# Kernel optimization log

Measured on AMD Instinct MI355X. Metric: run time of the kernel, lower is better.

Reference implementation:

```python
import jax, jax.numpy as jnp
import numpy as np

NUM_HEADS = 4

def _pos_encoding(seq_len, d, dtype):
    # standard sinusoidal positional encoding [seq_len, d]
    pos = jnp.arange(seq_len, dtype=jnp.float32)[:, None]
    i = jnp.arange(0, d, 2, dtype=jnp.float32)
    div = jnp.exp(-jnp.log(10000.0) * i / d)
    ang = pos * div
    pe = jnp.zeros((seq_len, d), jnp.float32)
    pe = pe.at[:, 0::2].set(jnp.sin(ang)).at[:, 1::2].set(jnp.cos(ang))
    return pe.astype(dtype)

def _layer_norm(x, g, b, eps=1e-5):
    m = jnp.mean(x, axis=-1, keepdims=True)
    v = jnp.mean(jnp.square(x - m), axis=-1, keepdims=True)
    return (x - m) / jnp.sqrt(v + eps) * g + b

def setup_inputs() -> dict:
    key = jax.random.key(0)
    ks = jax.random.split(key, 10)
    B, S, H, W, N = 8, 512, 768, 8, 4096
    s = 0.02
    token_reps = jax.random.normal(ks[0], (B, S, H), jnp.float32)
    starts = jax.random.randint(ks[1], (B, N), 0, S - W)
    widths = jax.random.randint(ks[2], (B, N), 1, W + 1)
    span_ids = jnp.stack([starts, starts + widths], axis=-1)  # end > start, end <= S
    span_masks = jax.random.randint(ks[3], (B, N), 0, 2)
    return dict(
        token_reps=token_reps,
        dummy_query=jax.random.normal(ks[4], (H,), jnp.float32) * s,
        in_proj_w=jax.random.normal(ks[5], (3 * H, H), jnp.float32) * s,
        in_proj_b=jnp.zeros((3 * H,), jnp.float32),
        out_w=jax.random.normal(ks[6], (H, H), jnp.float32) * s,
        out_b=jnp.zeros((H,), jnp.float32),
        ln_g=jnp.ones((H,), jnp.float32),
        ln_b=jnp.zeros((H,), jnp.float32),
        ffn_w1=jax.random.normal(ks[7], (H, 4 * H), jnp.float32) * s,
        ffn_b1=jnp.zeros((4 * H,), jnp.float32),
        ffn_w2=jax.random.normal(ks[8], (4 * H, H), jnp.float32) * s,
        ffn_b2=jnp.zeros((H,), jnp.float32),
        span_ids=span_ids,
        span_masks=span_masks,
    )

def reference(token_reps, dummy_query, in_proj_w, in_proj_b, out_w, out_b,
              ln_g, ln_b, ffn_w1, ffn_b1, ffn_w2, ffn_b2, span_ids, span_masks):
    B, S, H = token_reps.shape
    N = span_ids.shape[1]
    NH = NUM_HEADS
    DH = H // NH
    # sequence positional encoding (dropout is identity in eval mode)
    x = token_reps + _pos_encoding(S, H, token_reps.dtype)[None]
    Wq, Wk, Wv = jnp.split(in_proj_w, 3, axis=0)
    bq, bk, bv = jnp.split(in_proj_b, 3)
    # single shared dummy query -> per-head query [NH, DH]
    q = (dummy_query @ Wq.T + bq).reshape(NH, DH)
    k = (x @ Wk.T + bk).reshape(B, S, NH, DH)
    v = (x @ Wv.T + bv).reshape(B, S, NH, DH)
    # scores are identical across spans since the query is shared: [B, NH, S]
    scores = jnp.einsum('hd,bshd->bhs', q, k) / jnp.sqrt(jnp.asarray(DH, x.dtype))
    pos = jnp.arange(S)
    # per-span key validity: start <= pos < end, and span not masked out  [B, N, S]
    valid = (pos[None, None, :] >= span_ids[..., 0:1]) & \
            (pos[None, None, :] < span_ids[..., 1:2]) & \
            (span_masks[..., None] != 0)
    logits = jnp.where(valid[:, :, None, :], scores[:, None, :, :], -1e9)  # [B,N,NH,S]
    w = jax.nn.softmax(logits, axis=-1)
    attn = jnp.einsum('bnhs,bshd->bnhd', w, v).reshape(B, N, H)
    attn = attn @ out_w.T + out_b
    h1 = _layer_norm(attn + dummy_query, ln_g, ln_b)
    ffn = jax.nn.relu(h1 @ ffn_w1 + ffn_b1) @ ffn_w2 + ffn_b2
    out = _layer_norm(ffn + h1, ln_g, ln_b)
    # masked spans produce exact zeros, matching the original loop
    return out * (span_masks[..., None] != 0).astype(out.dtype)
```

## Files before the change

### kernel.cpp

```cpp
#include <hip/hip_runtime.h>
#include <hip/hip_bf16.h>

#define Bb 8
#define Ss 512
#define Hh 768
#define NHh 4
#define Nn 4096
#define ROWS (Bb * Nn)
#define SCB 128

typedef _Float16 f16x8 __attribute__((ext_vector_type(8)));
typedef _Float16 f16x4 __attribute__((ext_vector_type(4)));
typedef _Float16 f16x2 __attribute__((ext_vector_type(2)));
typedef float f32x4 __attribute__((ext_vector_type(4)));

#define DEVINL __device__ __forceinline__

DEVINL void gld_lds16(const void* g, void* l) {
  __builtin_amdgcn_global_load_lds(
      (const __attribute__((address_space(1))) void*)g,
      (__attribute__((address_space(3))) void*)l, 16, 0, 0);
}

template <int V>
DEVINL void wait_vmcnt() {
  if constexpr (V == 0) asm volatile("s_waitcnt vmcnt(0)" ::: "memory");
  else if constexpr (V == 3) asm volatile("s_waitcnt vmcnt(3)" ::: "memory");
  else if constexpr (V == 4) asm volatile("s_waitcnt vmcnt(4)" ::: "memory");
  else if constexpr (V == 6) asm volatile("s_waitcnt vmcnt(6)" ::: "memory");
  else if constexpr (V == 8) asm volatile("s_waitcnt vmcnt(8)" ::: "memory");
}

DEVINL float block_sum256(float v, float* red) {
#pragma unroll
  for (int o = 32; o; o >>= 1) v += __shfl_xor(v, o, 64);
  const int wid = threadIdx.x >> 6, lane = threadIdx.x & 63;
  if (lane == 0) red[wid] = v;
  __syncthreads();
  float r = red[0] + red[1] + red[2] + red[3];
  __syncthreads();
  return r;
}

__global__ __launch_bounds__(256) void x_kernel(const float* __restrict__ tok,
                                                _Float16* __restrict__ x) {
  int idx = blockIdx.x * 256 + threadIdx.x;
  int t = idx % 384;
  int bs = idx / 384;
  int s = bs & (Ss - 1);
  float div = expf(-(float)t * 0.02398526138535465f);
  float ang = (float)s * div;
  float sv = sinf(ang), cv = cosf(ang);
  const float2 tv = ((const float2*)tok)[(size_t)bs * 384 + t];
  f16x2 o;
  o[0] = (_Float16)(tv.x + sv);
  o[1] = (_Float16)(tv.y + cv);
  *(f16x2*)&x[(size_t)bs * Hh + 2 * t] = o;
}

__global__ __launch_bounds__(256) void q_kernel(const float* __restrict__ dq,
                                                const float* __restrict__ ipw,
                                                const float* __restrict__ ipb,
                                                float* __restrict__ qout) {
  __shared__ float red[4];
  int o = blockIdx.x;
  const float* wr = ipw + (size_t)o * Hh;
  float s = 0.f;
#pragma unroll
  for (int e = 0; e < 3; e++) {
    int j = threadIdx.x + 256 * e;
    s += dq[j] * wr[j];
  }
  s = block_sum256(s, red);
  if (threadIdx.x == 0) qout[o] = s + ipb[o];
}

__global__ __launch_bounds__(256) void c_kernel(const float* __restrict__ q,
                                                const float* __restrict__ ipw,
                                                const float* __restrict__ ipb,
                                                float* __restrict__ cout,
                                                float* __restrict__ sbias) {
  __shared__ float red[4];
  int bid = blockIdx.x;
  int t = threadIdx.x;
  if (bid < 3072) {
    int h = bid / Hh;
    int j = bid - h * Hh;
    float s = 0.f;
    if (t < 192) s = q[h * 192 + t] * ipw[(size_t)(Hh + h * 192 + t) * Hh + j];
    s = block_sum256(s, red);
    if (t == 0) cout[bid] = s;
  } else {
    int h = bid - 3072;
    float s = 0.f;
    if (t < 192) s = q[h * 192 + t] * ipb[Hh + h * 192 + t];
    s = block_sum256(s, red);
    if (t == 0) sbias[h] = s;
  }
}

__global__ __launch_bounds__(256) void score_kernel(
    const _Float16* __restrict__ x, const float* __restrict__ c,
    const float* __restrict__ sbias, float* __restrict__ scores) {
  int bs = blockIdx.x;
  int wid = threadIdx.x >> 6, lane = threadIdx.x & 63;
  const _Float16* xr = x + (size_t)bs * Hh;
  const float* ch = c + wid * Hh;
  float s = 0.f;
#pragma unroll
  for (int e = 0; e < 12; e++) {
    int j = e * 64 + lane;
    s += (float)xr[j] * ch[j];
  }
#pragma unroll
  for (int o = 32; o; o >>= 1) s += __shfl_xor(s, o, 64);
  if (lane == 0) {
    int b = bs >> 9, pos = bs & (Ss - 1);
    scores[((size_t)(b * NHh + wid)) * Ss + pos] =
        (s + sbias[wid]) * 0.07216878364870322f;
  }
}

__global__ __launch_bounds__(256) void cvt_kernel(const float* __restrict__ in,
                                                  _Float16* __restrict__ out) {
  int i = blockIdx.x * 256 + threadIdx.x;
  float4 f = ((const float4*)in)[i];
  f16x4 o;
  o[0] = (_Float16)f.x;
  o[1] = (_Float16)f.y;
  o[2] = (_Float16)f.z;
  o[3] = (_Float16)f.w;
  ((f16x4*)out)[i] = o;
}

__global__ __launch_bounds__(256) void trcvt_kernel(const float* __restrict__ in,
                                                    _Float16* __restrict__ out,
                                                    int R, int C) {
  __shared__ float tile[32][33];
  int c0 = blockIdx.x * 32, r0 = blockIdx.y * 32;
  int tx = threadIdx.x & 31, ty0 = threadIdx.x >> 5;
#pragma unroll
  for (int ty = ty0; ty < 32; ty += 8)
    tile[ty][tx] = in[(size_t)(r0 + ty) * C + c0 + tx];
  __syncthreads();
#pragma unroll
  for (int ty = ty0; ty < 32; ty += 8)
    out[(size_t)(c0 + ty) * R + r0 + tx] = (_Float16)tile[tx][ty];
}

__global__ __launch_bounds__(256) void scan1_kernel(const int* __restrict__ mask,
                                                    int* __restrict__ bsum) {
  int r = blockIdx.x * 256 + threadIdx.x;
  unsigned long long b = __ballot(mask[r] != 0);
  __shared__ int wsum[4];
  int lane = threadIdx.x & 63, wid = threadIdx.x >> 6;
  if (lane == 0) wsum[wid] = __popcll(b);
  __syncthreads();
  if (threadIdx.x == 0)
    bsum[blockIdx.x] = wsum[0] + wsum[1] + wsum[2] + wsum[3];
}
__global__ __launch_bounds__(64) void scan2_kernel(const int* __restrict__ bsum,
                                                   int* __restrict__ boff,
                                                   int* __restrict__ cnt) {
  if (threadIdx.x == 0) {
    int acc = 0;
    for (int i = 0; i < SCB; i++) {
      boff[i] = acc;
      acc += bsum[i];
    }
    *cnt = acc;
  }
}
__global__ __launch_bounds__(256) void cidx_kernel(const int* __restrict__ mask,
                                                   const int* __restrict__ boff,
                                                   int* __restrict__ cidx) {
  int r = blockIdx.x * 256 + threadIdx.x;
  int m = mask[r] != 0;
  unsigned long long b = __ballot(m);
  __shared__ int wsum[4];
  int lane = threadIdx.x & 63, wid = threadIdx.x >> 6;
  if (lane == 0) wsum[wid] = __popcll(b);
  __syncthreads();
  int pre = 0;
#pragma unroll
  for (int i = 0; i < 3; i++)
    if (i < wid) pre += wsum[i];
  pre += __popcll(b & ((1ULL << lane) - 1));
  if (m) cidx[r] = boff[blockIdx.x] + pre;
}

#define PIPE_LOOP(LPSV)                                   \
  const int nt = K >> 5;                                  \
  STAGE(0, 0);                                            \
  STAGE(1, 32);                                           \
  int t = 0;                                              \
  for (; t <= nt - 6; t += 3) {                           \
    wait_vmcnt<LPSV>();                                   \
    __builtin_amdgcn_s_barrier();                         \
    STAGE(2, (t + 2) * 32);                               \
    COMPUTE(0);                                           \
    wait_vmcnt<LPSV>();                                   \
    __builtin_amdgcn_s_barrier();                         \
    STAGE(0, (t + 3) * 32);                               \
    COMPUTE(1);                                           \
    wait_vmcnt<LPSV>();                                   \
    __builtin_amdgcn_s_barrier();                         \
    STAGE(1, (t + 4) * 32);                               \
    COMPUTE(2);                                           \
  }                                                       \
    \
  wait_vmcnt<LPSV>();                                     \
  __builtin_amdgcn_s_barrier();                           \
  STAGE(2, (nt - 1) * 32);                                \
  COMPUTE(0);                                             \
  wait_vmcnt<LPSV>();                                     \
  __builtin_amdgcn_s_barrier();                           \
  COMPUTE(1);                                             \
  wait_vmcnt<0>();                                        \
  __builtin_amdgcn_s_barrier();                           \
  COMPUTE(2);

template <int RELU, int BN>
__global__ __launch_bounds__(256, 2) void gemm_nt(
    const _Float16* __restrict__ A, const _Float16* __restrict__ W,
    const float* __restrict__ bias, _Float16* __restrict__ C, int N, int K,
    int nn, const int* __restrict__ mcount) {
  const int bid = (int)blockIdx.x;
  const int mi = (bid >> 3) / nn;
  const int nt_ = (bid >> 3) - mi * nn;
  const long m0 = (long)(mi * 8 + (bid & 7)) * 128;
  const long n0 = (long)nt_ * BN;
  if (mcount && m0 >= (long)*mcount) return;
  __shared__ __align__(16) _Float16 As[3][128 * 32];
  __shared__ __align__(16) _Float16 Bs[3][BN * 32];
  const int tid = threadIdx.x;
  const int wid = tid >> 6;
  const int lane = tid & 63;
  constexpr int LPS = (BN == 128) ? 4 : 3;

  const int c0 = wid * 64 + lane;
  const int c1 = c0 + 256;
  const int sw0 = ((c0 & 3) ^ ((c0 >> 3) & 3)) * 8;
  const int sw1 = ((c1 & 3) ^ ((c1 >> 3) & 3)) * 8;
  const _Float16* gA0 = A + (m0 + (c0 >> 2)) * K + sw0;
  const _Float16* gA1 = A + (m0 + (c1 >> 2)) * K + sw1;
  const _Float16* gB0 = W + (n0 + (c0 >> 2)) * K + sw0;
  const _Float16* gB1 = W + (n0 + (c1 >> 2)) * K + sw1;

  const int wr = (wid >> 1) * 64;
  const int wc = (wid & 1) * (BN / 2);
  constexpr int NF = BN / 32;
  const int fr = lane & 15;
  const int fkb = lane >> 4;

  f32x4 acc[4][NF];
#pragma unroll
  for (int mi2 = 0; mi2 < 4; mi2++)
#pragma unroll
    for (int ni = 0; ni < NF; ni++) acc[mi2][ni] = (f32x4){0.f, 0.f, 0.f, 0.f};

#define STAGE(buf, k0)                                                  \
  do {                                                                  \
    gld_lds16(gA0 + (k0), &As[buf][wid * 512]);                         \
    gld_lds16(gA1 + (k0), &As[buf][2048 + wid * 512]);                  \
    gld_lds16(gB0 + (k0), &Bs[buf][wid * 512]);                         \
    if constexpr (BN == 128) gld_lds16(gB1 + (k0), &Bs[buf][2048 + wid * 512]); \
  } while (0)

#define COMPUTE(buf)                                                          \
  do {                                                                        \
    f16x8 af[4], bf[NF];                                                      \
    _Pragma("unroll") for (int i = 0; i < 4; i++) {                           \
      int r_ = wr + i * 16 + fr;                                              \
      af[i] = *(const f16x8*)&As[buf][r_ * 32 + ((fkb ^ ((r_ >> 1) & 3)) * 8)]; \
    }                                                                         \
    _Pragma("unroll") for (int i = 0; i < NF; i++) {                          \
      int r_ = wc + i * 16 + fr;                                              \
      bf[i] = *(const f16x8*)&Bs[buf][r_ * 32 + ((fkb ^ ((r_ >> 1) & 3)) * 8)]; \
    }                                                                         \
    __builtin_amdgcn_s_setprio(1);                                            \
    _Pragma("unroll") for (int mi2 = 0; mi2 < 4; mi2++)                       \
        _Pragma("unroll") for (int ni = 0; ni < NF; ni++)                     \
            acc[mi2][ni] = __builtin_amdgcn_mfma_f32_16x16x32_f16(            \
                af[mi2], bf[ni], acc[mi2][ni], 0, 0, 0);                      \
    __builtin_amdgcn_s_setprio(0);                                            \
  } while (0)

  PIPE_LOOP(LPS)
#undef STAGE
#undef COMPUTE

  const int crow = (lane >> 4) * 4;
  const int ccol = lane & 15;
  float bv[NF];
#pragma unroll
  for (int ni = 0; ni < NF; ni++)
    bv[ni] = bias ? bias[n0 + wc + ni * 16 + ccol] : 0.f;
#pragma unroll
  for (int mi2 = 0; mi2 < 4; mi2++)
#pragma unroll
    for (int ni = 0; ni < NF; ni++)
#pragma unroll
      for (int i = 0; i < 4; i++) {
        float v = acc[mi2][ni][i] + bv[ni];
        if (RELU) v = fmaxf(v, 0.f);
        C[(m0 + wr + mi2 * 16 + crow + i) * (long)N + (n0 + wc + ni * 16 + ccol)] =
            (_Float16)v;
      }
}

template <int RELU>
__global__ __launch_bounds__(512, 4) void gemm8_nt(
    const _Float16* __restrict__ A, const _Float16* __restrict__ W,
    const float* __restrict__ bias, _Float16* __restrict__ C, int N, int K,
    int nn, const int* __restrict__ mcount) {
  const int bid = (int)blockIdx.x;
  const int mi = (bid >> 3) / nn;
  const int nt_ = (bid >> 3) - mi * nn;
  const long m0 = (long)(mi * 8 + (bid & 7)) * 256;
  const long n0 = (long)nt_ * 128;
  if (mcount && m0 >= (long)*mcount) return;
  __shared__ __align__(16) _Float16 As[3][256 * 32];
  __shared__ __align__(16) _Float16 Bs[3][128 * 32];
  const int tid = threadIdx.x;
  const int w = tid >> 6;
  const int lane = tid & 63;
  constexpr int LPS = 3;

  const int rA0 = w * 16 + (lane >> 2);
  const int rA1 = rA0 + 128;
  const int cb = lane & 3;
  const int swA0 = (cb ^ ((rA0 >> 1) & 3)) * 8;
  const int swA1 = (cb ^ ((rA1 >> 1) & 3)) * 8;
  const _Float16* gA0 = A + (m0 + rA0) * K + swA0;
  const _Float16* gA1 = A + (m0 + rA1) * K + swA1;
  const _Float16* gB0 = W + (n0 + rA0) * K + swA0;

  const int wr = (w >> 1) * 64;
  const int wc = (w & 1) * 64;
  const int fr = lane & 15;
  const int fkb = lane >> 4;

  f32x4 acc[4][4];
#pragma unroll
  for (int mi2 = 0; mi2 < 4; mi2++)
#pragma unroll
    for (int ni = 0; ni < 4; ni++) acc[mi2][ni] = (f32x4){0.f, 0.f, 0.f, 0.f};

#define STAGE(buf, k0)                                   \
  do {                                                   \
    gld_lds16(gA0 + (k0), &As[buf][w * 512]);            \
    gld_lds16(gA1 + (k0), &As[buf][(w + 8) * 512]);      \
    gld_lds16(gB0 + (k0), &Bs[buf][w * 512]);            \
  } while (0)

#define COMPUTE(buf)                                                          \
  do {                                                                        \
    f16x8 af[4], bf[4];                                                       \
    _Pragma("unroll") for (int i = 0; i < 4; i++) {                           \
      int r_ = wr + i * 16 + fr;                                              \
      af[i] = *(const f16x8*)&As[buf][r_ * 32 + ((fkb ^ ((r_ >> 1) & 3)) * 8)]; \
    }                                                                         \
    _Pragma("unroll") for (int i = 0; i < 4; i++) {                           \
      int r_ = wc + i * 16 + fr;                                              \
      bf[i] = *(const f16x8*)&Bs[buf][r_ * 32 + ((fkb ^ ((r_ >> 1) & 3)) * 8)]; \
    }                                                                         \
    __builtin_amdgcn_s_setprio(1);                                            \
    _Pragma("unroll") for (int mi2 = 0; mi2 < 4; mi2++)                       \
        _Pragma("unroll") for (int ni = 0; ni < 4; ni++)                      \
            acc[mi2][ni] = __builtin_amdgcn_mfma_f32_16x16x32_f16(            \
                af[mi2], bf[ni], acc[mi2][ni], 0, 0, 0);                      \
    __builtin_amdgcn_s_setprio(0);                                            \
  } while (0)

  PIPE_LOOP(LPS)
#undef STAGE
#undef COMPUTE

  const int crow = (lane >> 4) * 4;
  const int ccol = lane & 15;
  float bv[4];
#pragma unroll
  for (int ni = 0; ni < 4; ni++)
    bv[ni] = bias ? bias[n0 + wc + ni * 16 + ccol] : 0.f;
#pragma unroll
  for (int mi2 = 0; mi2 < 4; mi2++)
#pragma unroll
    for (int ni = 0; ni < 4; ni++)
#pragma unroll
      for (int i = 0; i < 4; i++) {
        float v = acc[mi2][ni][i] + bv[ni];
        if (RELU) v = fmaxf(v, 0.f);
        C[(m0 + wr + mi2 * 16 + crow + i) * (long)N + (n0 + wc + ni * 16 + ccol)] =
            (_Float16)v;
      }
}

__global__ __launch_bounds__(192) void pool_kernel(
    const _Float16* __restrict__ v, const float* __restrict__ scores,
    const int* __restrict__ span_ids, const int* __restrict__ span_masks,
    _Float16* __restrict__ attn, const int* __restrict__ cidx) {
  int r = blockIdx.x;
  if (span_masks[r] == 0) return;
  int slot = cidx[r];
  int i = threadIdx.x;
  int h = i / 48;
  int d0 = i * 4;
  int b = r >> 12;
  int st = span_ids[2 * r], en = span_ids[2 * r + 1];
  int wdt = en - st;
  const float* sc = scores + ((size_t)(b * NHh + h)) * Ss + st;
  float w[8];
  float mx = -1e30f;
#pragma unroll
  for (int j = 0; j < 8; j++) {
    float t = (j < wdt) ? sc[j] : -1e30f;
    w[j] = t;
    mx = fmaxf(mx, t);
  }
  float sum = 0.f;
#pragma unroll
  for (int j = 0; j < 8; j++) {
    float e = (j < wdt) ? expf(w[j] - mx) : 0.f;
    w[j] = e;
    sum += e;
  }
  float inv = 1.f / sum;
  float a0 = 0.f, a1 = 0.f, a2 = 0.f, a3 = 0.f;
#pragma unroll
  for (int j = 0; j < 8; j++) {
    if (j < wdt) {
      f16x4 vv = *(const f16x4*)(v + ((size_t)(b * Ss + st + j)) * Hh + d0);
      float wj = w[j] * inv;
      a0 += wj * (float)vv[0];
      a1 += wj * (float)vv[1];
      a2 += wj * (float)vv[2];
      a3 += wj * (float)vv[3];
    }
  }
  f16x4 o;
  o[0] = (_Float16)a0;
  o[1] = (_Float16)a1;
  o[2] = (_Float16)a2;
  o[3] = (_Float16)a3;
  *(f16x4*)&attn[(size_t)slot * Hh + d0] = o;
}

__global__ __launch_bounds__(256) void ln0_kernel(
    _Float16* __restrict__ X, const float* __restrict__ AddV,
    const float* __restrict__ g, const float* __restrict__ bta,
    const int* __restrict__ mcount) {
  __shared__ float red[4];
  int r = blockIdx.x;
  if (r >= *mcount) return;
  int t = threadIdx.x;
  float xv[3];
#pragma unroll
  for (int e = 0; e < 3; e++) {
    int d = t + 256 * e;
    xv[e] = (float)X[(size_t)r * Hh + d] + AddV[d];
  }
  float s = xv[0] + xv[1] + xv[2];
  s = block_sum256(s, red);
  float mean = s * (1.f / 768.f);
  float vs = 0.f;
#pragma unroll
  for (int e = 0; e < 3; e++) {
    float d = xv[e] - mean;
    vs += d * d;
  }
  vs = block_sum256(vs, red);
  float inv = rsqrtf(vs * (1.f / 768.f) + 1e-5f);
#pragma unroll
  for (int e = 0; e < 3; e++) {
    int d = t + 256 * e;
    X[(size_t)r * Hh + d] = (_Float16)((xv[e] - mean) * inv * g[d] + bta[d]);
  }
}

__global__ __launch_bounds__(256) void ln1_kernel(
    const _Float16* __restrict__ F2c, const _Float16* __restrict__ h1c,
    const int* __restrict__ cidx, const float* __restrict__ g,
    const float* __restrict__ bta, const int* __restrict__ mask,
    float* __restrict__ out) {
  __shared__ float red[4];
  int r = blockIdx.x;
  int t = threadIdx.x;
  float* orow = out + (size_t)r * Hh;
  if (mask[r] == 0) {
#pragma unroll
    for (int e = 0; e < 3; e++) orow[t + 256 * e] = 0.f;
    return;
  }
  int c = cidx[r];
  float xv[3];
#pragma unroll
  for (int e = 0; e < 3; e++) {
    int d = t + 256 * e;
    xv[e] = (float)F2c[(size_t)c * Hh + d] + (float)h1c[(size_t)c * Hh + d];
  }
  float s = xv[0] + xv[1] + xv[2];
  s = block_sum256(s, red);
  float mean = s * (1.f / 768.f);
  float vs = 0.f;
#pragma unroll
  for (int e = 0; e < 3; e++) {
    float d = xv[e] - mean;
    vs += d * d;
  }
  vs = block_sum256(vs, red);
  float inv = rsqrtf(vs * (1.f / 768.f) + 1e-5f);
#pragma unroll
  for (int e = 0; e < 3; e++) {
    int d = t + 256 * e;
    orow[d] = (xv[e] - mean) * inv * g[d] + bta[d];
  }
}

extern "C" void kernel_launch(void* const* d_in, const int* in_sizes, int n_in,
                              void* d_out, int out_size, void* d_ws,
                              size_t ws_size, hipStream_t stream) {
  (void)out_size;
  if (n_in != 14) return;
  if (in_sizes[0] != 3145728 || in_sizes[2] != 1769472 ||
      in_sizes[3] != 2304 || in_sizes[4] != 589824 ||
      in_sizes[8] != 2359296 || in_sizes[9] != 3072 ||
      in_sizes[12] != 65536 || in_sizes[13] != 32768)
    return;

  const float* tok   = (const float*)d_in[0];
  const float* dq    = (const float*)d_in[1];
  const float* ipw   = (const float*)d_in[2];
  const float* ipb   = (const float*)d_in[3];
  const float* outw  = (const float*)d_in[4];
  const float* outb  = (const float*)d_in[5];
  const float* lng   = (const float*)d_in[6];
  const float* lnb   = (const float*)d_in[7];
  const float* w1    = (const float*)d_in[8];
  const float* b1    = (const float*)d_in[9];
  const float* w2    = (const float*)d_in[10];
  const float* b2    = (const float*)d_in[11];
  const int* spid    = (const int*)d_in[12];
  const int* spmask  = (const int*)d_in[13];

  char* ws = (char*)d_ws;
  size_t off = 0;
  auto alloc = [&](size_t bytes) {
    size_t r = off;
    off = (off + bytes + 255) & ~(size_t)255;
    return r;
  };
  _Float16* X16  = (_Float16*)(ws + alloc((size_t)Bb * Ss * Hh * 2));
  float* SC      = (float*)(ws + alloc((size_t)Bb * NHh * Ss * 4));
  float* Q       = (float*)(ws + alloc(768 * 4));
  float* Cc      = (float*)(ws + alloc(3072 * 4));
  float* SB      = (float*)(ws + alloc(4 * 4));
  _Float16* WV16 = (_Float16*)(ws + alloc((size_t)768 * 768 * 2));
  _Float16* OW16 = (_Float16*)(ws + alloc((size_t)768 * 768 * 2));
  _Float16* WT1  = (_Float16*)(ws + alloc((size_t)3072 * 768 * 2));
  _Float16* WT2  = (_Float16*)(ws + alloc((size_t)768 * 3072 * 2));
  _Float16* ATTN = (_Float16*)(ws + alloc((size_t)ROWS * Hh * 2));
  _Float16* PROJ = (_Float16*)(ws + alloc((size_t)ROWS * Hh * 2));
  _Float16* F1   = (_Float16*)(ws + alloc((size_t)ROWS * 3072 * 2));
  if (ws_size < off) return;
  _Float16* F2 = ATTN;

  int* CIDX = (int*)X16;
  int* BSUM = (int*)X16 + ROWS;
  int* BOFF = (int*)X16 + ROWS + SCB;
  int* CNT  = (int*)X16 + ROWS + 2 * SCB;

  _Float16* V16 = (_Float16*)d_out;

  cvt_kernel<<<576, 256, 0, stream>>>(ipw + (size_t)1536 * 768, WV16);
  cvt_kernel<<<576, 256, 0, stream>>>(outw, OW16);
  trcvt_kernel<<<dim3(96, 24), 256, 0, stream>>>(w1, WT1, 768, 3072);
  trcvt_kernel<<<dim3(24, 96), 256, 0, stream>>>(w2, WT2, 3072, 768);

  x_kernel<<<(Bb * Ss * 384) / 256, 256, 0, stream>>>(tok, X16);
  q_kernel<<<768, 256, 0, stream>>>(dq, ipw, ipb, Q);
  c_kernel<<<3076, 256, 0, stream>>>(Q, ipw, ipb, Cc, SB);
  score_kernel<<<Bb * Ss, 256, 0, stream>>>(X16, Cc, SB, SC);
  gemm_nt<0, 64><<<384, 256, 0, stream>>>(X16, WV16, ipb + 1536, V16,
                                          768, 768, 12, nullptr);
  scan1_kernel<<<SCB, 256, 0, stream>>>(spmask, BSUM);
  scan2_kernel<<<1, 64, 0, stream>>>(BSUM, BOFF, CNT);
  cidx_kernel<<<SCB, 256, 0, stream>>>(spmask, BOFF, CIDX);
  pool_kernel<<<ROWS, 192, 0, stream>>>(V16, SC, spid, spmask, ATTN, CIDX);
  gemm8_nt<0><<<768, 512, 0, stream>>>(ATTN, OW16, outb, PROJ,
                                       768, 768, 6, CNT);
  ln0_kernel<<<ROWS, 256, 0, stream>>>(PROJ, dq, lng, lnb, CNT);
  gemm8_nt<1><<<3072, 512, 0, stream>>>(PROJ, WT1, b1, F1,
                                        3072, 768, 24, CNT);
  gemm8_nt<0><<<768, 512, 0, stream>>>(F1, WT2, b2, F2,
                                       768, 3072, 6, CNT);
  ln1_kernel<<<ROWS, 256, 0, stream>>>(F2, PROJ, CIDX, lng, lnb, spmask,
                                       (float*)d_out);
}
```

Baseline: 372.2 us.

## Split-K the narrow GEMMs, chunk the FFN over rows, restructure the LDS pipeline

The out-projection and FFN2 GEMMs, which have only 768 output columns, now use a two-way split-K. The grid doubles, and each half writes a partial fp16 result to its own buffer. The partials are summed inside the following layer-norm kernels. The FFN runs in two row chunks of 16384 rows so the F1 intermediate buffer is halved and more likely to stay in cache. The software pipeline now prefetches three stages and restages each buffer after computing it. This adds fp16 partial-sum rounding, extra launches, and another barrier per iteration.

```diff
diff --git a/kernel.cpp b/kernel.cpp
--- a/kernel.cpp
+++ b/kernel.cpp
@@ -8,6 +8,7 @@
 #define Nn 4096
 #define ROWS (Bb * Nn)
 #define SCB 128
+#define CHROWS 16384
 
 typedef _Float16 f16x8 __attribute__((ext_vector_type(8)));
 typedef _Float16 f16x4 __attribute__((ext_vector_type(4)));
@@ -189,35 +190,33 @@
   if (m) cidx[r] = boff[blockIdx.x] + pre;
 }
 
-#define PIPE_LOOP(LPSV)                                   \
-  const int nt = K >> 5;                                  \
-  STAGE(0, 0);                                            \
-  STAGE(1, 32);                                           \
-  int t = 0;                                              \
-  for (; t <= nt - 6; t += 3) {                           \
-    wait_vmcnt<LPSV>();                                   \
-    __builtin_amdgcn_s_barrier();                         \
-    STAGE(2, (t + 2) * 32);                               \
-    COMPUTE(0);                                           \
-    wait_vmcnt<LPSV>();                                   \
-    __builtin_amdgcn_s_barrier();                         \
-    STAGE(0, (t + 3) * 32);                               \
-    COMPUTE(1);                                           \
-    wait_vmcnt<LPSV>();                                   \
-    __builtin_amdgcn_s_barrier();                         \
-    STAGE(1, (t + 4) * 32);                               \
-    COMPUTE(2);                                           \
-  }                                                       \
-    \
-  wait_vmcnt<LPSV>();                                     \
-  __builtin_amdgcn_s_barrier();                           \
-  STAGE(2, (nt - 1) * 32);                                \
-  COMPUTE(0);                                             \
-  wait_vmcnt<LPSV>();                                     \
-  __builtin_amdgcn_s_barrier();                           \
-  COMPUTE(1);                                             \
-  wait_vmcnt<0>();                                        \
-  __builtin_amdgcn_s_barrier();                           \
+#define ITER_RESTAGE(b, knext)              \
+  do {                                      \
+    wait_vmcnt<2 * LPS>();                  \
+    __builtin_amdgcn_s_barrier();           \
+    COMPUTE(b);                             \
+    __builtin_amdgcn_s_barrier();           \
+    STAGE(b, (knext));                      \
+  } while (0)
+#define PIPE_MAIN()                         \
+  const int nt = KK >> 5;                   \
+  STAGE(0, 0);                              \
+  STAGE(1, 32);                             \
+  STAGE(2, 64);                             \
+  int t = 0;                                \
+  for (; t <= nt - 6; t += 3) {             \
+    ITER_RESTAGE(0, (t + 3) * 32);          \
+    ITER_RESTAGE(1, (t + 4) * 32);          \
+    ITER_RESTAGE(2, (t + 5) * 32);          \
+  }                                         \
+  wait_vmcnt<2 * LPS>();                    \
+  __builtin_amdgcn_s_barrier();             \
+  COMPUTE(0);                               \
+  wait_vmcnt<LPS>();                        \
+  __builtin_amdgcn_s_barrier();             \
+  COMPUTE(1);                               \
+  wait_vmcnt<0>();                          \
+  __builtin_amdgcn_s_barrier();             \
   COMPUTE(2);
 
 template <int RELU, int BN>
@@ -237,6 +236,7 @@
   const int wid = tid >> 6;
   const int lane = tid & 63;
   constexpr int LPS = (BN == 128) ? 4 : 3;
+  const int KK = K;
 
   const int c0 = wid * 64 + lane;
   const int c1 = c0 + 256;
@@ -286,7 +286,7 @@
     __builtin_amdgcn_s_setprio(0);                                            \
   } while (0)
 
-  PIPE_LOOP(LPS)
+  PIPE_MAIN()
 #undef STAGE
 #undef COMPUTE
 
@@ -309,17 +309,29 @@
       }
 }
 
-template <int RELU>
+template <int RELU, int SPLIT>
 __global__ __launch_bounds__(512, 4) void gemm8_nt(
     const _Float16* __restrict__ A, const _Float16* __restrict__ W,
-    const float* __restrict__ bias, _Float16* __restrict__ C, int N, int K,
-    int nn, const int* __restrict__ mcount) {
-  const int bid = (int)blockIdx.x;
+    const float* __restrict__ bias, _Float16* __restrict__ C0,
+    _Float16* __restrict__ C1, int N, int K, int nn, int mbase,
+    const int* __restrict__ mcount) {
+  int bid = (int)blockIdx.x;
+  int half = 0;
+  if constexpr (SPLIT == 2) {
+    const int hg = (int)gridDim.x >> 1;
+    half = bid >= hg;
+    bid -= half * hg;
+  }
   const int mi = (bid >> 3) / nn;
   const int nt_ = (bid >> 3) - mi * nn;
   const long m0 = (long)(mi * 8 + (bid & 7)) * 256;
   const long n0 = (long)nt_ * 128;
-  if (mcount && m0 >= (long)*mcount) return;
+  if (mcount && (long)mbase + m0 >= (long)*mcount) return;
+  const int KK = K / SPLIT;
+  const int koff = half * KK;
+  _Float16* C = half ? C1 : C0;
+  const float* biasp = (SPLIT == 2 && half == 1) ? nullptr : bias;
+
   __shared__ __align__(16) _Float16 As[3][256 * 32];
   __shared__ __align__(16) _Float16 Bs[3][128 * 32];
   const int tid = threadIdx.x;
@@ -332,9 +344,9 @@
   const int cb = lane & 3;
   const int swA0 = (cb ^ ((rA0 >> 1) & 3)) * 8;
   const int swA1 = (cb ^ ((rA1 >> 1) & 3)) * 8;
-  const _Float16* gA0 = A + (m0 + rA0) * K + swA0;
-  const _Float16* gA1 = A + (m0 + rA1) * K + swA1;
-  const _Float16* gB0 = W + (n0 + rA0) * K + swA0;
+  const _Float16* gA0 = A + (m0 + rA0) * K + koff + swA0;
+  const _Float16* gA1 = A + (m0 + rA1) * K + koff + swA1;
+  const _Float16* gB0 = W + (n0 + rA0) * K + koff + swA0;
 
   const int wr = (w >> 1) * 64;
   const int wc = (w & 1) * 64;
@@ -373,7 +385,7 @@
     __builtin_amdgcn_s_setprio(0);                                            \
   } while (0)
 
-  PIPE_LOOP(LPS)
+  PIPE_MAIN()
 #undef STAGE
 #undef COMPUTE
 
@@ -382,7 +394,7 @@
   float bv[4];
 #pragma unroll
   for (int ni = 0; ni < 4; ni++)
-    bv[ni] = bias ? bias[n0 + wc + ni * 16 + ccol] : 0.f;
+    bv[ni] = biasp ? biasp[n0 + wc + ni * 16 + ccol] : 0.f;
 #pragma unroll
   for (int mi2 = 0; mi2 < 4; mi2++)
 #pragma unroll
@@ -447,9 +459,9 @@
 }
 
 __global__ __launch_bounds__(256) void ln0_kernel(
-    _Float16* __restrict__ X, const float* __restrict__ AddV,
-    const float* __restrict__ g, const float* __restrict__ bta,
-    const int* __restrict__ mcount) {
+    _Float16* __restrict__ XA, const _Float16* __restrict__ XB,
+    const float* __restrict__ AddV, const float* __restrict__ g,
+    const float* __restrict__ bta, const int* __restrict__ mcount) {
   __shared__ float red[4];
   int r = blockIdx.x;
   if (r >= *mcount) return;
@@ -458,7 +470,8 @@
 #pragma unroll
   for (int e = 0; e < 3; e++) {
     int d = t + 256 * e;
-    xv[e] = (float)X[(size_t)r * Hh + d] + AddV[d];
+    xv[e] = (float)XA[(size_t)r * Hh + d] + (float)XB[(size_t)r * Hh + d] +
+            AddV[d];
   }
   float s = xv[0] + xv[1] + xv[2];
   s = block_sum256(s, red);
@@ -474,15 +487,15 @@
 #pragma unroll
   for (int e = 0; e < 3; e++) {
     int d = t + 256 * e;
-    X[(size_t)r * Hh + d] = (_Float16)((xv[e] - mean) * inv * g[d] + bta[d]);
+    XA[(size_t)r * Hh + d] = (_Float16)((xv[e] - mean) * inv * g[d] + bta[d]);
   }
 }
 
 __global__ __launch_bounds__(256) void ln1_kernel(
-    const _Float16* __restrict__ F2c, const _Float16* __restrict__ h1c,
-    const int* __restrict__ cidx, const float* __restrict__ g,
-    const float* __restrict__ bta, const int* __restrict__ mask,
-    float* __restrict__ out) {
+    const _Float16* __restrict__ F2a, const _Float16* __restrict__ F2b,
+    const _Float16* __restrict__ h1c, const int* __restrict__ cidx,
+    const float* __restrict__ g, const float* __restrict__ bta,
+    const int* __restrict__ mask, float* __restrict__ out) {
   __shared__ float red[4];
   int r = blockIdx.x;
   int t = threadIdx.x;
@@ -497,7 +510,8 @@
 #pragma unroll
   for (int e = 0; e < 3; e++) {
     int d = t + 256 * e;
-    xv[e] = (float)F2c[(size_t)c * Hh + d] + (float)h1c[(size_t)c * Hh + d];
+    xv[e] = (float)F2a[(size_t)c * Hh + d] + (float)F2b[(size_t)c * Hh + d] +
+            (float)h1c[(size_t)c * Hh + d];
   }
   float s = xv[0] + xv[1] + xv[2];
   s = block_sum256(s, red);
@@ -561,9 +575,11 @@
   _Float16* WT2  = (_Float16*)(ws + alloc((size_t)768 * 3072 * 2));
   _Float16* ATTN = (_Float16*)(ws + alloc((size_t)ROWS * Hh * 2));
   _Float16* PROJ = (_Float16*)(ws + alloc((size_t)ROWS * Hh * 2));
-  _Float16* F1   = (_Float16*)(ws + alloc((size_t)ROWS * 3072 * 2));
+  _Float16* PB   = (_Float16*)(ws + alloc((size_t)ROWS * Hh * 2));
+  _Float16* F1   = (_Float16*)(ws + alloc((size_t)CHROWS * 3072 * 2));
   if (ws_size < off) return;
-  _Float16* F2 = ATTN;
+  _Float16* F2A = ATTN;
+  _Float16* F2B = PB;
 
   int* CIDX = (int*)X16;
   int* BSUM = (int*)X16 + ROWS;
@@ -587,13 +603,17 @@
   scan2_kernel<<<1, 64, 0, stream>>>(BSUM, BOFF, CNT);
   cidx_kernel<<<SCB, 256, 0, stream>>>(spmask, BOFF, CIDX);
   pool_kernel<<<ROWS, 192, 0, stream>>>(V16, SC, spid, spmask, ATTN, CIDX);
-  gemm8_nt<0><<<768, 512, 0, stream>>>(ATTN, OW16, outb, PROJ,
-                                       768, 768, 6, CNT);
-  ln0_kernel<<<ROWS, 256, 0, stream>>>(PROJ, dq, lng, lnb, CNT);
-  gemm8_nt<1><<<3072, 512, 0, stream>>>(PROJ, WT1, b1, F1,
-                                        3072, 768, 24, CNT);
-  gemm8_nt<0><<<768, 512, 0, stream>>>(F1, WT2, b2, F2,
-                                       768, 3072, 6, CNT);
-  ln1_kernel<<<ROWS, 256, 0, stream>>>(F2, PROJ, CIDX, lng, lnb, spmask,
+  gemm8_nt<0, 2><<<1536, 512, 0, stream>>>(ATTN, OW16, outb, PROJ, PB,
+                                           768, 768, 6, 0, CNT);
+  ln0_kernel<<<ROWS, 256, 0, stream>>>(PROJ, PB, dq, lng, lnb, CNT);
+  for (int ch = 0; ch < 2; ch++) {
+    const int mb = ch * CHROWS;
+    gemm8_nt<1, 1><<<1536, 512, 0, stream>>>(
+        PROJ + (size_t)mb * Hh, WT1, b1, F1, nullptr, 3072, 768, 24, mb, CNT);
+    gemm8_nt<0, 2><<<768, 512, 0, stream>>>(
+        F1, WT2, b2, F2A + (size_t)mb * Hh, F2B + (size_t)mb * Hh,
+        768, 3072, 6, mb, CNT);
+  }
+  ln1_kernel<<<ROWS, 256, 0, stream>>>(F2A, F2B, PROJ, CIDX, lng, lnb, spmask,
                                        (float*)d_out);
 }
```

After: 414.9 us. 1.11x slower.
